# Kernel tuning notes

Hardware: AMD Instinct MI355X
Metric: run time of the kernel (lower is better)

Reference implementation:

```python
import jax, jax.numpy as jnp
import numpy as np

D = 8388608  # vector_dim
N = 1024     # phase table size
M = 1024     # magnitude table size


def setup_inputs() -> dict:
    key = jax.random.key(0)
    k1, k2, k3, k4 = jax.random.split(key, 4)
    ctx_phase_idx = jax.random.randint(k1, (D,), 0, N, dtype=jnp.int64)
    ctx_mag_idx = jax.random.randint(k2, (D,), 0, M, dtype=jnp.int64)
    self_phase_idx = jax.random.randint(k3, (D,), 0, N, dtype=jnp.int64)
    self_mag_idx = jax.random.randint(k4, (D,), 0, M, dtype=jnp.int64)
    # Lookup tables (the ExtendedLookupTableModule's precomputed tables):
    # phase table = cos(2*pi*i/N), its grad = -sin(2*pi*i/N) * (2*pi/N)
    # magnitude table = exp(linspace), its grad = same exp * slope
    phase_grid = 2.0 * jnp.pi * jnp.arange(N, dtype=jnp.float32) / N
    mag_grid = jnp.linspace(-1.0, 1.0, M, dtype=jnp.float32)
    cos_table = jnp.cos(phase_grid)
    cos_grad_table = -jnp.sin(phase_grid) * (2.0 * jnp.pi / N)
    exp_table = jnp.exp(mag_grid)
    exp_grad_table = exp_table * (2.0 / (M - 1))
    return {
        "ctx_phase_idx": ctx_phase_idx,
        "ctx_mag_idx": ctx_mag_idx,
        "self_phase_idx": self_phase_idx,
        "self_mag_idx": self_mag_idx,
        "cos_table": cos_table,
        "exp_table": exp_table,
        "cos_grad_table": cos_grad_table,
        "exp_grad_table": exp_grad_table,
    }


def reference(ctx_phase_idx, ctx_mag_idx, self_phase_idx, self_mag_idx,
              cos_table, exp_table, cos_grad_table, exp_grad_table):
    # mod-indexed sums
    phase_out = (ctx_phase_idx + self_phase_idx) % N  # [D] int
    mag_out = (ctx_mag_idx + self_mag_idx) % M        # [D] int
    # four table gathers
    cos_vals = cos_table[phase_out]       # [D]
    exp_vals = exp_table[mag_out]         # [D]
    dcos = cos_grad_table[phase_out]      # [D]
    dexp = exp_grad_table[mag_out]        # [D]
    # elementwise multiplies + reduction
    signal = cos_vals * exp_vals          # [D]
    grad_phase = dcos * exp_vals          # [D]
    grad_mag = cos_vals * dexp            # [D]
    strength = signal.sum()
    return (phase_out, mag_out, signal, strength, grad_phase, grad_mag)
```

## Files before the change

kernel.cpp:

```cpp
#include <hip/hip_runtime.h>

constexpr int D_TOTAL = 8388608;
constexpr int TBL = 1024;
constexpr int IDX_MASK = 1023;
constexpr int BLOCK = 256;
constexpr int VEC = 8;
constexpr int ELEMS_PER_BLOCK = BLOCK * VEC;
constexpr int NBLOCKS = D_TOTAL / ELEMS_PER_BLOCK;

typedef float f32x4 __attribute__((ext_vector_type(4)));
typedef float f32x8 __attribute__((ext_vector_type(8)));
typedef int   i32x8 __attribute__((ext_vector_type(8)));
typedef f32x4 f32x4u __attribute__((aligned(4)));
typedef f32x8 f32x8u __attribute__((aligned(4)));

__global__ __launch_bounds__(BLOCK) void phasecell_main(
    const int* __restrict__ ctx_p, const int* __restrict__ ctx_m,
    const int* __restrict__ self_p, const int* __restrict__ self_m,
    const float* __restrict__ cos_t, const float* __restrict__ exp_t,
    const float* __restrict__ dcos_t, const float* __restrict__ dexp_t,
    float* __restrict__ out, float* __restrict__ block_sums) {
  const int base = (blockIdx.x * BLOCK + threadIdx.x) * VEC;

  const i32x8 cp = *reinterpret_cast<const i32x8*>(ctx_p + base);
  const i32x8 cm = *reinterpret_cast<const i32x8*>(ctx_m + base);
  const i32x8 sp = *reinterpret_cast<const i32x8*>(self_p + base);
  const i32x8 sm = *reinterpret_cast<const i32x8*>(self_m + base);

  __shared__ float2 s_phase[TBL];
  __shared__ float2 s_mag[TBL];
  for (int i = threadIdx.x; i < TBL; i += BLOCK) {
    s_phase[i] = make_float2(cos_t[i], dcos_t[i]);
    s_mag[i]   = make_float2(exp_t[i], dexp_t[i]);
  }
  __syncthreads();

  int p[VEC], m[VEC];
#pragma unroll
  for (int j = 0; j < VEC; ++j) {
    p[j] = (cp[j] + sp[j]) & IDX_MASK;
    m[j] = (cm[j] + sm[j]) & IDX_MASK;
  }

  f32x8 po, mo;
#pragma unroll
  for (int j = 0; j < VEC; ++j) {
    po[j] = (float)p[j];
    mo[j] = (float)m[j];
  }
  __builtin_nontemporal_store(po, reinterpret_cast<f32x8*>(out + base));
  __builtin_nontemporal_store(mo, reinterpret_cast<f32x8*>(out + D_TOTAL + base));

  float* sig_base = out + 2 * D_TOTAL + base;
  float* gp_base  = out + 3 * D_TOTAL + 1 + base;
  float* gm_base  = out + 4 * D_TOTAL + 1 + base;

  f32x8 sg;
  f32x8u gp, gm;
  float local = 0.f;
#pragma unroll
  for (int j = 0; j < VEC; ++j) {
    const float2 ph = s_phase[p[j]];
    const float2 mg = s_mag[m[j]];
    sg[j] = ph.x * mg.x;
    gp[j] = ph.y * mg.x;
    gm[j] = ph.x * mg.y;
    local += sg[j];
  }

  __builtin_nontemporal_store(sg, reinterpret_cast<f32x8*>(sig_base));
  *reinterpret_cast<f32x8u*>(gp_base) = gp;
  *reinterpret_cast<f32x8u*>(gm_base) = gm;

#pragma unroll
  for (int off = 32; off > 0; off >>= 1) local += __shfl_down(local, off, 64);
  __shared__ float wsum[BLOCK / 64];
  const int wave = threadIdx.x >> 6;
  const int lane = threadIdx.x & 63;
  if (lane == 0) wsum[wave] = local;
  __syncthreads();
  if (threadIdx.x == 0) {
    float t = 0.f;
#pragma unroll
    for (int w = 0; w < BLOCK / 64; ++w) t += wsum[w];
    block_sums[blockIdx.x] = t;
  }
}

__global__ __launch_bounds__(BLOCK) void phasecell_reduce(
    const float* __restrict__ partials, float* __restrict__ strength_out) {
  float s = 0.f;
  for (int i = threadIdx.x; i < NBLOCKS; i += BLOCK) s += partials[i];
#pragma unroll
  for (int off = 32; off > 0; off >>= 1) s += __shfl_down(s, off, 64);
  __shared__ float wsum[BLOCK / 64];
  const int wave = threadIdx.x >> 6;
  const int lane = threadIdx.x & 63;
  if (lane == 0) wsum[wave] = s;
  __syncthreads();
  if (threadIdx.x == 0) {
    float t = 0.f;
#pragma unroll
    for (int w = 0; w < BLOCK / 64; ++w) t += wsum[w];
    strength_out[0] = t;
  }
}

extern "C" void kernel_launch(void* const* d_in, const int* in_sizes, int n_in,
                              void* d_out, int out_size, void* d_ws, size_t ws_size,
                              hipStream_t stream) {
  const int* ctx_p  = (const int*)d_in[0];
  const int* ctx_m  = (const int*)d_in[1];
  const int* self_p = (const int*)d_in[2];
  const int* self_m = (const int*)d_in[3];
  const float* cos_t  = (const float*)d_in[4];
  const float* exp_t  = (const float*)d_in[5];
  const float* dcos_t = (const float*)d_in[6];
  const float* dexp_t = (const float*)d_in[7];
  float* out = (float*)d_out;
  float* block_sums = (float*)d_ws;

  phasecell_main<<<NBLOCKS, BLOCK, 0, stream>>>(
      ctx_p, ctx_m, self_p, self_m, cos_t, exp_t, dcos_t, dexp_t, out, block_sums);
  phasecell_reduce<<<1, BLOCK, 0, stream>>>(block_sums, out + 3 * (size_t)D_TOTAL);
}
```

Before: 308.5 us.

## Process two tiles per block to amortize LDS table staging; use plain stores

Each block now handles two 2048-element tiles, so the 16 KB shared-memory table fill and its barrier are paid once per two tiles instead of once per tile. The loads for the second tile are issued after the barrier. The non-temporal stores for indices and signal are replaced with ordinary vector stores. Per-tile partial sums are still written separately, so the reduction layout is unchanged. The cost is higher register pressure and half as many blocks in flight.

```diff
diff --git a/kernel.cpp b/kernel.cpp
--- a/kernel.cpp
+++ b/kernel.cpp
@@ -5,14 +5,48 @@
 constexpr int IDX_MASK = 1023;
 constexpr int BLOCK = 256;
 constexpr int VEC = 8;
-constexpr int ELEMS_PER_BLOCK = BLOCK * VEC;
-constexpr int NBLOCKS = D_TOTAL / ELEMS_PER_BLOCK;
+constexpr int ELEMS_PER_TILE = BLOCK * VEC;
+constexpr int NTILES = D_TOTAL / ELEMS_PER_TILE;
+constexpr int TPB = 2;
+constexpr int NBLOCKS_MAIN = NTILES / TPB;
 
 typedef float f32x4 __attribute__((ext_vector_type(4)));
 typedef float f32x8 __attribute__((ext_vector_type(8)));
 typedef int   i32x8 __attribute__((ext_vector_type(8)));
-typedef f32x4 f32x4u __attribute__((aligned(4)));
 typedef f32x8 f32x8u __attribute__((aligned(4)));
+
+__device__ __forceinline__ float process_tile(
+    int base, i32x8 cp, i32x8 cm, i32x8 sp, i32x8 sm,
+    const float2* __restrict__ s_phase, const float2* __restrict__ s_mag,
+    float* __restrict__ out) {
+  int p[VEC], m[VEC];
+#pragma unroll
+  for (int j = 0; j < VEC; ++j) {
+    p[j] = (cp[j] + sp[j]) & IDX_MASK;
+    m[j] = (cm[j] + sm[j]) & IDX_MASK;
+  }
+  f32x8 po, mo, sg;
+  f32x8u gp, gm;
+  float local = 0.f;
+#pragma unroll
+  for (int j = 0; j < VEC; ++j) {
+    const float2 ph = s_phase[p[j]];
+    const float2 mg = s_mag[m[j]];
+    const float s = ph.x * mg.x;
+    sg[j] = s;
+    gp[j] = ph.y * mg.x;
+    gm[j] = ph.x * mg.y;
+    po[j] = (float)p[j];
+    mo[j] = (float)m[j];
+    local += s;
+  }
+  *reinterpret_cast<f32x8*>(out + base)                     = po;
+  *reinterpret_cast<f32x8*>(out + D_TOTAL + base)           = mo;
+  *reinterpret_cast<f32x8*>(out + 2 * D_TOTAL + base)       = sg;
+  *reinterpret_cast<f32x8u*>(out + 3 * D_TOTAL + 1 + base)  = gp;
+  *reinterpret_cast<f32x8u*>(out + 4 * D_TOTAL + 1 + base)  = gm;
+  return local;
+}
 
 __global__ __launch_bounds__(BLOCK) void phasecell_main(
     const int* __restrict__ ctx_p, const int* __restrict__ ctx_m,
@@ -20,12 +54,13 @@
     const float* __restrict__ cos_t, const float* __restrict__ exp_t,
     const float* __restrict__ dcos_t, const float* __restrict__ dexp_t,
     float* __restrict__ out, float* __restrict__ block_sums) {
-  const int base = (blockIdx.x * BLOCK + threadIdx.x) * VEC;
+  const int base0 = (blockIdx.x * TPB) * ELEMS_PER_TILE + threadIdx.x * VEC;
+  const int base1 = base0 + ELEMS_PER_TILE;
 
-  const i32x8 cp = *reinterpret_cast<const i32x8*>(ctx_p + base);
-  const i32x8 cm = *reinterpret_cast<const i32x8*>(ctx_m + base);
-  const i32x8 sp = *reinterpret_cast<const i32x8*>(self_p + base);
-  const i32x8 sm = *reinterpret_cast<const i32x8*>(self_m + base);
+  const i32x8 cp0 = *reinterpret_cast<const i32x8*>(ctx_p + base0);
+  const i32x8 cm0 = *reinterpret_cast<const i32x8*>(ctx_m + base0);
+  const i32x8 sp0 = *reinterpret_cast<const i32x8*>(self_p + base0);
+  const i32x8 sm0 = *reinterpret_cast<const i32x8*>(self_m + base0);
 
   __shared__ float2 s_phase[TBL];
   __shared__ float2 s_mag[TBL];
@@ -35,62 +70,41 @@
   }
   __syncthreads();
 
-  int p[VEC], m[VEC];
-#pragma unroll
-  for (int j = 0; j < VEC; ++j) {
-    p[j] = (cp[j] + sp[j]) & IDX_MASK;
-    m[j] = (cm[j] + sm[j]) & IDX_MASK;
-  }
+  const i32x8 cp1 = *reinterpret_cast<const i32x8*>(ctx_p + base1);
+  const i32x8 cm1 = *reinterpret_cast<const i32x8*>(ctx_m + base1);
+  const i32x8 sp1 = *reinterpret_cast<const i32x8*>(self_p + base1);
+  const i32x8 sm1 = *reinterpret_cast<const i32x8*>(self_m + base1);
 
-  f32x8 po, mo;
-#pragma unroll
-  for (int j = 0; j < VEC; ++j) {
-    po[j] = (float)p[j];
-    mo[j] = (float)m[j];
-  }
-  __builtin_nontemporal_store(po, reinterpret_cast<f32x8*>(out + base));
-  __builtin_nontemporal_store(mo, reinterpret_cast<f32x8*>(out + D_TOTAL + base));
-
-  float* sig_base = out + 2 * D_TOTAL + base;
-  float* gp_base  = out + 3 * D_TOTAL + 1 + base;
-  float* gm_base  = out + 4 * D_TOTAL + 1 + base;
-
-  f32x8 sg;
-  f32x8u gp, gm;
-  float local = 0.f;
-#pragma unroll
-  for (int j = 0; j < VEC; ++j) {
-    const float2 ph = s_phase[p[j]];
-    const float2 mg = s_mag[m[j]];
-    sg[j] = ph.x * mg.x;
-    gp[j] = ph.y * mg.x;
-    gm[j] = ph.x * mg.y;
-    local += sg[j];
-  }
-
-  __builtin_nontemporal_store(sg, reinterpret_cast<f32x8*>(sig_base));
-  *reinterpret_cast<f32x8u*>(gp_base) = gp;
-  *reinterpret_cast<f32x8u*>(gm_base) = gm;
-
-#pragma unroll
-  for (int off = 32; off > 0; off >>= 1) local += __shfl_down(local, off, 64);
-  __shared__ float wsum[BLOCK / 64];
+  __shared__ float wsum[TPB][BLOCK / 64];
   const int wave = threadIdx.x >> 6;
   const int lane = threadIdx.x & 63;
-  if (lane == 0) wsum[wave] = local;
+
+  float r0 = process_tile(base0, cp0, cm0, sp0, sm0, s_phase, s_mag, out);
+#pragma unroll
+  for (int off = 32; off > 0; off >>= 1) r0 += __shfl_down(r0, off, 64);
+  if (lane == 0) wsum[0][wave] = r0;
+
+  float r1 = process_tile(base1, cp1, cm1, sp1, sm1, s_phase, s_mag, out);
+#pragma unroll
+  for (int off = 32; off > 0; off >>= 1) r1 += __shfl_down(r1, off, 64);
+  if (lane == 0) wsum[1][wave] = r1;
+
   __syncthreads();
   if (threadIdx.x == 0) {
-    float t = 0.f;
+    float t0 = 0.f, t1 = 0.f;
 #pragma unroll
-    for (int w = 0; w < BLOCK / 64; ++w) t += wsum[w];
-    block_sums[blockIdx.x] = t;
+    for (int w = 0; w < BLOCK / 64; ++w) t0 += wsum[0][w];
+#pragma unroll
+    for (int w = 0; w < BLOCK / 64; ++w) t1 += wsum[1][w];
+    block_sums[blockIdx.x * TPB]     = t0;
+    block_sums[blockIdx.x * TPB + 1] = t1;
   }
 }
 
 __global__ __launch_bounds__(BLOCK) void phasecell_reduce(
     const float* __restrict__ partials, float* __restrict__ strength_out) {
   float s = 0.f;
-  for (int i = threadIdx.x; i < NBLOCKS; i += BLOCK) s += partials[i];
+  for (int i = threadIdx.x; i < NTILES; i += BLOCK) s += partials[i];
 #pragma unroll
   for (int off = 32; off > 0; off >>= 1) s += __shfl_down(s, off, 64);
   __shared__ float wsum[BLOCK / 64];
@@ -120,7 +134,7 @@
   float* out = (float*)d_out;
   float* block_sums = (float*)d_ws;
 
-  phasecell_main<<<NBLOCKS, BLOCK, 0, stream>>>(
+  phasecell_main<<<NBLOCKS_MAIN, BLOCK, 0, stream>>>(
       ctx_p, ctx_m, self_p, self_m, cos_t, exp_t, dcos_t, dexp_t, out, block_sums);
   phasecell_reduce<<<1, BLOCK, 0, stream>>>(block_sums, out + 3 * (size_t)D_TOTAL);
 }
```

Measured after the change: 292.5 us. 1.05x faster.
